# Performance work log

Hardware: AMD Instinct MI355X
Metric: run time of the kernel (lower is better)

The kernel has to match this reference:

```python
import jax, jax.numpy as jnp
import numpy as np

HIDDEN = 2048
HEADS = 16
HEAD_DIM = HIDDEN // HEADS  # 128
SCALE = 1.0 / np.sqrt(HEAD_DIM).astype(np.float32)


def setup_inputs() -> dict:
    key = jax.random.key(0)
    k1, k2, k3, k4, k5 = jax.random.split(key, 5)
    B, QL = 8, 1024
    NB, BS = 32, 128  # num_blocks, block_size -> kv_len = 4096
    query = jax.random.normal(k1, (B, QL, HIDDEN), dtype=jnp.float32)
    kv_k = jax.random.normal(k2, (NB, BS, HIDDEN), dtype=jnp.float32)
    kv_v = jax.random.normal(k3, (NB, BS, HIDDEN), dtype=jnp.float32)
    # nn.Linear(bias=False) weights: y = x @ W.T
    Wq = jax.random.normal(k4, (HIDDEN, HIDDEN), dtype=jnp.float32) * (1.0 / np.sqrt(HIDDEN))
    Wo = jax.random.normal(k5, (HIDDEN, HIDDEN), dtype=jnp.float32) * (1.0 / np.sqrt(HIDDEN))
    return {"query": query, "kv_k": kv_k, "kv_v": kv_v, "Wq": Wq, "Wo": Wo}


def reference(query, kv_k, kv_v, Wq, Wo):
    # query: [B, QL, H*D]; kv_k/kv_v: [NB, BS, H*D] (shared across batch,
    # NOT re-projected in the paged path, matching the torch module).
    B, QL, _ = query.shape
    NB, BS, _ = kv_k.shape
    KV = NB * BS
    Q = (query @ Wq.T).reshape(B, QL, HEADS, HEAD_DIM)          # bqhd
    K = kv_k.reshape(KV, HEADS, HEAD_DIM)                        # khd
    V = kv_v.reshape(KV, HEADS, HEAD_DIM)
    # Blockwise online-softmax over equal blocks == one stable softmax over kv.
    scores = jnp.einsum("bqhd,khd->bhqk", Q, K) * SCALE          # [B,H,QL,KV]
    attn = jax.nn.softmax(scores, axis=-1)
    out = jnp.einsum("bhqk,khd->bqhd", attn, V).reshape(B, QL, HIDDEN)
    return out @ Wo.T
```

## Files before the change

kernel.cpp:

```cpp
#include <hip/hip_runtime.h>

#define HIDDEN 2048
#define HEADS 16
#define HDIM 128
#define BQ 8
#define QLEN 1024
#define KVLEN 4096
#define MROWS (BQ * QLEN)

typedef __bf16 bf16x8 __attribute__((ext_vector_type(8)));
typedef float f32x4 __attribute__((ext_vector_type(4)));
typedef unsigned short u16;
typedef u16 u16x8 __attribute__((ext_vector_type(8)));
typedef float f32x8v __attribute__((ext_vector_type(8)));

__device__ __forceinline__ u16 f2bf(float f) {
  union { float f; unsigned u; } v; v.f = f;
  unsigned r = (v.u + 0x7FFFu + ((v.u >> 16) & 1u)) >> 16;
  return (u16)r;
}

__device__ __forceinline__ void async_ld16(const void* g, void* l) {
  __builtin_amdgcn_global_load_lds(
      (const __attribute__((address_space(1))) void*)g,
      (__attribute__((address_space(3))) void*)l, 16, 0, 0);
}

__global__ void convert_bf16(const float* __restrict__ src, u16* __restrict__ dst,
                             long n) {
  long base = ((long)blockIdx.x * blockDim.x + threadIdx.x) * 8;
  long stride = (long)gridDim.x * blockDim.x * 8;
  for (long i = base; i < n; i += stride) {
    f32x8v s = *(const f32x8v*)(src + i);
    u16x8 o;
#pragma unroll
    for (int j = 0; j < 8; j++) o[j] = f2bf(s[j]);
    *(u16x8*)(dst + i) = o;
  }
}

__global__ __launch_bounds__(256) void transpose_v(const float* __restrict__ V,
                                                   u16* __restrict__ Vt) {
  __shared__ u16 T[128][129];
  const int kv0 = blockIdx.x * 128;
  const int h = blockIdx.y;
  const int tid = threadIdx.x;
#pragma unroll
  for (int p = 0; p < 8; p++) {
    int idx = p * 2048 + tid * 8;
    int r = idx >> 7, c = idx & 127;
    f32x8v s = *(const f32x8v*)(V + (size_t)(kv0 + r) * HIDDEN + h * HDIM + c);
#pragma unroll
    for (int j = 0; j < 8; j++) T[r][c + j] = f2bf(s[j]);
  }
  __syncthreads();
#pragma unroll
  for (int p = 0; p < 8; p++) {
    int idx = p * 2048 + tid * 8;
    int d = idx >> 7, kv = idx & 127;
    u16x8 o;
#pragma unroll
    for (int j = 0; j < 8; j++) o[j] = T[kv + j][d];
    *(u16x8*)(Vt + ((size_t)h * HDIM + d) * KVLEN + kv0 + kv) = o;
  }
}

__global__ __launch_bounds__(256) void gemm_bt(
    const u16* __restrict__ A, const u16* __restrict__ Bt, void* __restrict__ C,
    int M, int N, int K, int outf) {
  __shared__ __align__(16) u16 Asm[4 * 128 * 8];
  __shared__ __align__(16) u16 Bsm[4 * 128 * 8];
  const int tid = threadIdx.x;
  const int wid = tid >> 6, lane = tid & 63;
  const int quad = lane >> 4, l15 = lane & 15;
  const int wm = wid >> 1, wn = wid & 1;
  const int lin = blockIdx.y * gridDim.x + blockIdx.x;
  const int cpx = (gridDim.x * gridDim.y) >> 3;
  const int swz = (lin & 7) * cpx + (lin >> 3);
  const int by = swz / gridDim.x;
  const int bx = swz - by * gridDim.x;
  const int row0 = by * 128;
  const int col0 = bx * 128;

  f32x4 acc[4][4];
#pragma unroll
  for (int i = 0; i < 4; i++)
#pragma unroll
    for (int j = 0; j < 4; j++) acc[i][j] = (f32x4){0.f, 0.f, 0.f, 0.f};

  for (int k0 = 0; k0 < K; k0 += 32) {
    __syncthreads();
#pragma unroll
    for (int i = 0; i < 4; i++) {
      int seg = wid + 4 * i;
      int isB = seg >> 3;
      int s = seg & 7;
      int q = s >> 1, hv = s & 1;
      const u16* gsrc = isB ? Bt : A;
      int grow = (isB ? col0 : row0) + hv * 64 + lane;
      const u16* g = gsrc + (size_t)grow * K + (k0 + q * 8);
      u16* l = (isB ? Bsm : Asm) + (q * 128 + hv * 64) * 8;
      async_ld16(g, l);
    }
    __syncthreads();
    bf16x8 af[4], bfr[4];
#pragma unroll
    for (int mt = 0; mt < 4; mt++)
      af[mt] = *(const bf16x8*)(Asm + (quad * 128 + wm * 64 + mt * 16 + l15) * 8);
#pragma unroll
    for (int nt = 0; nt < 4; nt++)
      bfr[nt] = *(const bf16x8*)(Bsm + (quad * 128 + wn * 64 + nt * 16 + l15) * 8);
#pragma unroll
    for (int mt = 0; mt < 4; mt++)
#pragma unroll
      for (int nt = 0; nt < 4; nt++)
        acc[mt][nt] = __builtin_amdgcn_mfma_f32_16x16x32_bf16(af[mt], bfr[nt], acc[mt][nt], 0, 0, 0);
  }

#pragma unroll
  for (int mt = 0; mt < 4; mt++)
#pragma unroll
    for (int r = 0; r < 4; r++) {
      int row = row0 + wm * 64 + mt * 16 + quad * 4 + r;
#pragma unroll
      for (int nt = 0; nt < 4; nt++) {
        int col = col0 + wn * 64 + nt * 16 + l15;
        if (outf) {
          ((float*)C)[(size_t)row * N + col] = acc[mt][nt][r];
        } else {
          ((u16*)C)[(size_t)row * N + col] = f2bf(acc[mt][nt][r]);
        }
      }
    }
}

__global__ __launch_bounds__(256, 2) void attn(
    const u16* __restrict__ Q,
    const u16* __restrict__ Kv,
    const u16* __restrict__ Vt,
    u16* __restrict__ O) {
  __shared__ __align__(16) u16 KVb[16 * 1024];
  __shared__ __align__(16) u16 Pb[128 * 136];
  const int tid = threadIdx.x;
  const int wid = tid >> 6, lane = tid & 63;
  const int quad = lane >> 4, l15 = lane & 15;
  const int lin = blockIdx.x + (blockIdx.y << 3) + (blockIdx.z << 7);
  const int swz = ((lin & 7) << 7) + (lin >> 3);
  const int h = swz >> 6, b = (swz >> 3) & 7, qt = swz & 7;
  const int qrow0 = b * QLEN + qt * 128;
  const int hcol = h * HDIM;
  const float cexp = 0.08838834764831845f * 1.4426950408889634f;

  bf16x8 qf[2][4];
#pragma unroll
  for (int mt = 0; mt < 2; mt++)
#pragma unroll
    for (int ks = 0; ks < 4; ks++) {
      int row = qrow0 + wid * 32 + mt * 16 + l15;
      qf[mt][ks] = *(const bf16x8*)(Q + (size_t)row * HIDDEN + hcol + ks * 32 + quad * 8);
    }

  f32x4 o[2][8];
#pragma unroll
  for (int mt = 0; mt < 2; mt++)
#pragma unroll
    for (int dt = 0; dt < 8; dt++) o[mt][dt] = (f32x4){0.f, 0.f, 0.f, 0.f};
  float mrun[2][4], lrun[2][4];
#pragma unroll
  for (int mt = 0; mt < 2; mt++)
#pragma unroll
    for (int r = 0; r < 4; r++) { mrun[mt][r] = -INFINITY; lrun[mt][r] = 0.f; }

  for (int kv0 = 0; kv0 < KVLEN; kv0 += 128) {
    __syncthreads();
#pragma unroll
    for (int i = 0; i < 8; i++) {
      int seg = wid + 4 * i;
      int ch = seg >> 1, sh = seg & 1;
      int kvr = kv0 + sh * 64 + lane;
      const u16* g = Kv + (size_t)kvr * HIDDEN + hcol + ch * 8;
      async_ld16(g, KVb + (ch * 128 + sh * 64) * 8);
    }
    __syncthreads();

    f32x4 sc[2][8];
#pragma unroll
    for (int mt = 0; mt < 2; mt++)
#pragma unroll
      for (int nt = 0; nt < 8; nt++) sc[mt][nt] = (f32x4){0.f, 0.f, 0.f, 0.f};
#pragma unroll
    for (int ks = 0; ks < 4; ks++) {
      bf16x8 kf[8];
#pragma unroll
      for (int nt = 0; nt < 8; nt++)
        kf[nt] = *(const bf16x8*)(KVb + ((ks * 4 + quad) * 128 + nt * 16 + l15) * 8);
#pragma unroll
      for (int mt = 0; mt < 2; mt++)
#pragma unroll
        for (int nt = 0; nt < 8; nt++)
          sc[mt][nt] = __builtin_amdgcn_mfma_f32_16x16x32_bf16(qf[mt][ks], kf[nt], sc[mt][nt], 0, 0, 0);
    }
    __syncthreads();

#pragma unroll
    for (int i = 0; i < 8; i++) {
      int seg = wid + 4 * i;
      int ch = seg >> 1, dh = seg & 1;
      int d = dh * 64 + lane;
      const u16* g = Vt + ((size_t)hcol + d) * KVLEN + kv0 + ch * 8;
      async_ld16(g, KVb + (ch * 128 + dh * 64) * 8);
    }

#pragma unroll
    for (int mt = 0; mt < 2; mt++) {
#pragma unroll
      for (int r = 0; r < 4; r++) {
        float mx = sc[mt][0][r];
#pragma unroll
        for (int nt = 1; nt < 8; nt++) mx = fmaxf(mx, sc[mt][nt][r]);
#pragma unroll
        for (int off = 1; off < 16; off <<= 1) mx = fmaxf(mx, __shfl_xor(mx, off, 64));
        float mn = fmaxf(mrun[mt][r], mx);
        float al = __builtin_amdgcn_exp2f((mrun[mt][r] - mn) * cexp);
        mrun[mt][r] = mn;
        float mc = mn * cexp;
        float ps = 0.f;
#pragma unroll
        for (int nt = 0; nt < 8; nt++) {
          float p = __builtin_amdgcn_exp2f(sc[mt][nt][r] * cexp - mc);
          sc[mt][nt][r] = p;
          ps += p;
        }
#pragma unroll
        for (int off = 1; off < 16; off <<= 1) ps += __shfl_xor(ps, off, 64);
        lrun[mt][r] = lrun[mt][r] * al + ps;
#pragma unroll
        for (int dt = 0; dt < 8; dt++) o[mt][dt][r] *= al;
      }
    }

#pragma unroll
    for (int mt = 0; mt < 2; mt++)
#pragma unroll
      for (int nt = 0; nt < 8; nt++)
#pragma unroll
        for (int r = 0; r < 4; r++) {
          int prow = wid * 32 + mt * 16 + quad * 4 + r;
          Pb[prow * 136 + nt * 16 + l15] = f2bf(sc[mt][nt][r]);
        }
    __syncthreads();

#pragma unroll
    for (int ks = 0; ks < 4; ks++) {
      bf16x8 pf[2], vf[8];
#pragma unroll
      for (int mt = 0; mt < 2; mt++)
        pf[mt] = *(const bf16x8*)(Pb + (wid * 32 + mt * 16 + l15) * 136 + ks * 32 + quad * 8);
#pragma unroll
      for (int dt = 0; dt < 8; dt++)
        vf[dt] = *(const bf16x8*)(KVb + ((ks * 4 + quad) * 128 + dt * 16 + l15) * 8);
#pragma unroll
      for (int mt = 0; mt < 2; mt++)
#pragma unroll
        for (int dt = 0; dt < 8; dt++)
          o[mt][dt] = __builtin_amdgcn_mfma_f32_16x16x32_bf16(pf[mt], vf[dt], o[mt][dt], 0, 0, 0);
    }
  }

#pragma unroll
  for (int mt = 0; mt < 2; mt++)
#pragma unroll
    for (int r = 0; r < 4; r++) {
      float inv = 1.0f / lrun[mt][r];
      int row = qrow0 + wid * 32 + mt * 16 + quad * 4 + r;
#pragma unroll
      for (int dt = 0; dt < 8; dt++) {
        int col = hcol + dt * 16 + l15;
        O[(size_t)row * HIDDEN + col] = f2bf(o[mt][dt][r] * inv);
      }
    }
}

extern "C" void kernel_launch(void* const* d_in, const int* in_sizes, int n_in,
                              void* d_out, int out_size, void* d_ws, size_t ws_size,
                              hipStream_t stream) {
  const float* query = (const float*)d_in[0];
  const float* kv_k  = (const float*)d_in[1];
  const float* kv_v  = (const float*)d_in[2];
  const float* Wq    = (const float*)d_in[3];
  const float* Wo    = (const float*)d_in[4];
  float* out = (float*)d_out;

  const long NQ = (long)MROWS * HIDDEN;
  const long NK = (long)KVLEN * HIDDEN;
  const long NW = (long)HIDDEN * HIDDEN;

  dim3 blk(256);

  u16* convQ  = (u16*)d_ws;
  u16* convK  = convQ + NQ;
  u16* Vtb    = convK + NK;
  u16* convWq = Vtb + NK;
  u16* convWo = convWq + NW;
  u16* Qws    = convWo + NW;
  u16* Ows    = convQ;

  convert_bf16<<<dim3((NQ / 8 + 255) / 256), blk, 0, stream>>>(query, convQ,  NQ);
  convert_bf16<<<dim3((NK / 8 + 255) / 256), blk, 0, stream>>>(kv_k,  convK,  NK);
  transpose_v<<<dim3(KVLEN / 128, HEADS), blk, 0, stream>>>(kv_v, Vtb);
  convert_bf16<<<dim3((NW / 8 + 255) / 256), blk, 0, stream>>>(Wq,    convWq, NW);
  convert_bf16<<<dim3((NW / 8 + 255) / 256), blk, 0, stream>>>(Wo,    convWo, NW);

  gemm_bt<<<dim3(HIDDEN / 128, MROWS / 128), blk, 0, stream>>>(convQ, convWq, Qws, MROWS, HIDDEN, HIDDEN, 0);
  attn<<<dim3(QLEN / 128, HEADS, BQ), blk, 0, stream>>>(Qws, convK, Vtb, Ows);
  gemm_bt<<<dim3(HIDDEN / 128, MROWS / 128), blk, 0, stream>>>(Ows, convWo, out, MROWS, HIDDEN, HIDDEN, 1);
}
```

Before: 1.048 ms.

## Split attention work across eight waves with sixteen query rows each

The attention kernel moves from 4 waves handling 32 query rows each to 8 waves (512 threads) handling 16 rows each, keeping the 128-row query tile per block. Per-thread register use for scores and output accumulators is halved, which allows higher occupancy (launch bounds 512,4), and the K/V tile loads are spread over more waves. The cost is that each K/V fragment read from LDS now feeds half as many MFMAs, doubling LDS read traffic per FLOP, and barriers synchronise more waves.

```diff
diff --git a/kernel.cpp b/kernel.cpp
--- a/kernel.cpp
+++ b/kernel.cpp
@@ -134,7 +134,7 @@
     }
 }
 
-__global__ __launch_bounds__(256, 2) void attn(
+__global__ __launch_bounds__(512, 4) void attn(
     const u16* __restrict__ Q,
     const u16* __restrict__ Kv,
     const u16* __restrict__ Vt,
@@ -151,31 +151,25 @@
   const int hcol = h * HDIM;
   const float cexp = 0.08838834764831845f * 1.4426950408889634f;
 
-  bf16x8 qf[2][4];
-#pragma unroll
-  for (int mt = 0; mt < 2; mt++)
-#pragma unroll
-    for (int ks = 0; ks < 4; ks++) {
-      int row = qrow0 + wid * 32 + mt * 16 + l15;
-      qf[mt][ks] = *(const bf16x8*)(Q + (size_t)row * HIDDEN + hcol + ks * 32 + quad * 8);
-    }
-
-  f32x4 o[2][8];
-#pragma unroll
-  for (int mt = 0; mt < 2; mt++)
-#pragma unroll
-    for (int dt = 0; dt < 8; dt++) o[mt][dt] = (f32x4){0.f, 0.f, 0.f, 0.f};
-  float mrun[2][4], lrun[2][4];
-#pragma unroll
-  for (int mt = 0; mt < 2; mt++)
-#pragma unroll
-    for (int r = 0; r < 4; r++) { mrun[mt][r] = -INFINITY; lrun[mt][r] = 0.f; }
+  bf16x8 qf[4];
+#pragma unroll
+  for (int ks = 0; ks < 4; ks++) {
+    int row = qrow0 + wid * 16 + l15;
+    qf[ks] = *(const bf16x8*)(Q + (size_t)row * HIDDEN + hcol + ks * 32 + quad * 8);
+  }
+
+  f32x4 o[8];
+#pragma unroll
+  for (int dt = 0; dt < 8; dt++) o[dt] = (f32x4){0.f, 0.f, 0.f, 0.f};
+  float mrun[4], lrun[4];
+#pragma unroll
+  for (int r = 0; r < 4; r++) { mrun[r] = -INFINITY; lrun[r] = 0.f; }
 
   for (int kv0 = 0; kv0 < KVLEN; kv0 += 128) {
     __syncthreads();
 #pragma unroll
-    for (int i = 0; i < 8; i++) {
-      int seg = wid + 4 * i;
+    for (int i = 0; i < 4; i++) {
+      int seg = wid + 8 * i;
       int ch = seg >> 1, sh = seg & 1;
       int kvr = kv0 + sh * 64 + lane;
       const u16* g = Kv + (size_t)kvr * HIDDEN + hcol + ch * 8;
@@ -183,11 +177,9 @@
     }
     __syncthreads();
 
-    f32x4 sc[2][8];
-#pragma unroll
-    for (int mt = 0; mt < 2; mt++)
-#pragma unroll
-      for (int nt = 0; nt < 8; nt++) sc[mt][nt] = (f32x4){0.f, 0.f, 0.f, 0.f};
+    f32x4 sc[8];
+#pragma unroll
+    for (int nt = 0; nt < 8; nt++) sc[nt] = (f32x4){0.f, 0.f, 0.f, 0.f};
 #pragma unroll
     for (int ks = 0; ks < 4; ks++) {
       bf16x8 kf[8];
@@ -195,16 +187,14 @@
       for (int nt = 0; nt < 8; nt++)
         kf[nt] = *(const bf16x8*)(KVb + ((ks * 4 + quad) * 128 + nt * 16 + l15) * 8);
 #pragma unroll
-      for (int mt = 0; mt < 2; mt++)
-#pragma unroll
-        for (int nt = 0; nt < 8; nt++)
-          sc[mt][nt] = __builtin_amdgcn_mfma_f32_16x16x32_bf16(qf[mt][ks], kf[nt], sc[mt][nt], 0, 0, 0);
-    }
-    __syncthreads();
-
-#pragma unroll
-    for (int i = 0; i < 8; i++) {
-      int seg = wid + 4 * i;
+      for (int nt = 0; nt < 8; nt++)
+        sc[nt] = __builtin_amdgcn_mfma_f32_16x16x32_bf16(qf[ks], kf[nt], sc[nt], 0, 0, 0);
+    }
+    __syncthreads();
+
+#pragma unroll
+    for (int i = 0; i < 4; i++) {
+      int seg = wid + 8 * i;
       int ch = seg >> 1, dh = seg & 1;
       int d = dh * 64 + lane;
       const u16* g = Vt + ((size_t)hcol + d) * KVLEN + kv0 + ch * 8;
@@ -212,73 +202,62 @@
     }
 
 #pragma unroll
-    for (int mt = 0; mt < 2; mt++) {
+    for (int r = 0; r < 4; r++) {
+      float mx = sc[0][r];
+#pragma unroll
+      for (int nt = 1; nt < 8; nt++) mx = fmaxf(mx, sc[nt][r]);
+#pragma unroll
+      for (int off = 1; off < 16; off <<= 1) mx = fmaxf(mx, __shfl_xor(mx, off, 64));
+      float mn = fmaxf(mrun[r], mx);
+      float al = __builtin_amdgcn_exp2f((mrun[r] - mn) * cexp);
+      mrun[r] = mn;
+      float mc = mn * cexp;
+      float ps = 0.f;
+#pragma unroll
+      for (int nt = 0; nt < 8; nt++) {
+        float p = __builtin_amdgcn_exp2f(sc[nt][r] * cexp - mc);
+        sc[nt][r] = p;
+        ps += p;
+      }
+#pragma unroll
+      for (int off = 1; off < 16; off <<= 1) ps += __shfl_xor(ps, off, 64);
+      lrun[r] = lrun[r] * al + ps;
+#pragma unroll
+      for (int dt = 0; dt < 8; dt++) o[dt][r] *= al;
+    }
+
+#pragma unroll
+    for (int nt = 0; nt < 8; nt++)
 #pragma unroll
       for (int r = 0; r < 4; r++) {
-        float mx = sc[mt][0][r];
-#pragma unroll
-        for (int nt = 1; nt < 8; nt++) mx = fmaxf(mx, sc[mt][nt][r]);
-#pragma unroll
-        for (int off = 1; off < 16; off <<= 1) mx = fmaxf(mx, __shfl_xor(mx, off, 64));
-        float mn = fmaxf(mrun[mt][r], mx);
-        float al = __builtin_amdgcn_exp2f((mrun[mt][r] - mn) * cexp);
-        mrun[mt][r] = mn;
-        float mc = mn * cexp;
-        float ps = 0.f;
-#pragma unroll
-        for (int nt = 0; nt < 8; nt++) {
-          float p = __builtin_amdgcn_exp2f(sc[mt][nt][r] * cexp - mc);
-          sc[mt][nt][r] = p;
-          ps += p;
-        }
-#pragma unroll
-        for (int off = 1; off < 16; off <<= 1) ps += __shfl_xor(ps, off, 64);
-        lrun[mt][r] = lrun[mt][r] * al + ps;
-#pragma unroll
-        for (int dt = 0; dt < 8; dt++) o[mt][dt][r] *= al;
+        int prow = wid * 16 + quad * 4 + r;
+        Pb[prow * 136 + nt * 16 + l15] = f2bf(sc[nt][r]);
       }
-    }
-
-#pragma unroll
-    for (int mt = 0; mt < 2; mt++)
-#pragma unroll
-      for (int nt = 0; nt < 8; nt++)
-#pragma unroll
-        for (int r = 0; r < 4; r++) {
-          int prow = wid * 32 + mt * 16 + quad * 4 + r;
-          Pb[prow * 136 + nt * 16 + l15] = f2bf(sc[mt][nt][r]);
-        }
     __syncthreads();
 
 #pragma unroll
     for (int ks = 0; ks < 4; ks++) {
-      bf16x8 pf[2], vf[8];
-#pragma unroll
-      for (int mt = 0; mt < 2; mt++)
-        pf[mt] = *(const bf16x8*)(Pb + (wid * 32 + mt * 16 + l15) * 136 + ks * 32 + quad * 8);
+      bf16x8 pf, vf[8];
+      pf = *(const bf16x8*)(Pb + (wid * 16 + l15) * 136 + ks * 32 + quad * 8);
 #pragma unroll
       for (int dt = 0; dt < 8; dt++)
         vf[dt] = *(const bf16x8*)(KVb + ((ks * 4 + quad) * 128 + dt * 16 + l15) * 8);
 #pragma unroll
-      for (int mt = 0; mt < 2; mt++)
-#pragma unroll
-        for (int dt = 0; dt < 8; dt++)
-          o[mt][dt] = __builtin_amdgcn_mfma_f32_16x16x32_bf16(pf[mt], vf[dt], o[mt][dt], 0, 0, 0);
-    }
-  }
-
-#pragma unroll
-  for (int mt = 0; mt < 2; mt++)
-#pragma unroll
-    for (int r = 0; r < 4; r++) {
-      float inv = 1.0f / lrun[mt][r];
-      int row = qrow0 + wid * 32 + mt * 16 + quad * 4 + r;
-#pragma unroll
-      for (int dt = 0; dt < 8; dt++) {
-        int col = hcol + dt * 16 + l15;
-        O[(size_t)row * HIDDEN + col] = f2bf(o[mt][dt][r] * inv);
-      }
-    }
+      for (int dt = 0; dt < 8; dt++)
+        o[dt] = __builtin_amdgcn_mfma_f32_16x16x32_bf16(pf, vf[dt], o[dt], 0, 0, 0);
+    }
+  }
+
+#pragma unroll
+  for (int r = 0; r < 4; r++) {
+    float inv = 1.0f / lrun[r];
+    int row = qrow0 + wid * 16 + quad * 4 + r;
+#pragma unroll
+    for (int dt = 0; dt < 8; dt++) {
+      int col = hcol + dt * 16 + l15;
+      O[(size_t)row * HIDDEN + col] = f2bf(o[dt][r] * inv);
+    }
+  }
 }
 
 extern "C" void kernel_launch(void* const* d_in, const int* in_sizes, int n_in,
@@ -312,6 +291,6 @@
   convert_bf16<<<dim3((NW / 8 + 255) / 256), blk, 0, stream>>>(Wo,    convWo, NW);
 
   gemm_bt<<<dim3(HIDDEN / 128, MROWS / 128), blk, 0, stream>>>(convQ, convWq, Qws, MROWS, HIDDEN, HIDDEN, 0);
-  attn<<<dim3(QLEN / 128, HEADS, BQ), blk, 0, stream>>>(Qws, convK, Vtb, Ows);
+  attn<<<dim3(QLEN / 128, HEADS, BQ), dim3(512), 0, stream>>>(Qws, convK, Vtb, Ows);
   gemm_bt<<<dim3(HIDDEN / 128, MROWS / 128), blk, 0, stream>>>(Ows, convWo, out, MROWS, HIDDEN, HIDDEN, 1);
 }
```

Result: no change. 1.042 ms (-0.5%).
